# Kernel optimization log

Measured on AMD Instinct MI355X. Metric: run time of the kernel, lower is better.

Reference implementation:

```python
import jax, jax.numpy as jnp
import numpy as np

BINS = 10  # constructor default


def setup_inputs() -> dict:
    key = jax.random.key(0)
    k1, k2 = jax.random.split(key)
    bs, cla = 262144, 128
    # probabilities strictly inside (0,1) so log terms are finite
    u = jax.random.uniform(k1, (bs, cla), dtype=jnp.float32)
    inputs = 0.01 + 0.98 * u
    # binary 0/1 targets as floats
    targets = jnp.round(jax.random.uniform(k2, (bs, cla), dtype=jnp.float32))
    return {"inputs": inputs, "targets": targets}


def reference(inputs, targets):
    bins = BINS
    tot = jnp.asarray(inputs.size, jnp.float32)  # bs * cla

    # gradient-norm proxy g = |p.detach() - t|, in [0, 1]
    g = jnp.abs(jax.lax.stop_gradient(inputs) - targets)

    # edges are i/bins with the last edge nudged to 1+1e-6, so
    # floor(g*bins) clipped to bins-1 reproduces the per-bin masks exactly
    idx = jnp.clip(jnp.floor(g * bins).astype(jnp.int32), 0, bins - 1)

    # histogram counts per bin (fused scatter-add instead of the Python loop)
    counts = jnp.zeros((bins,), jnp.float32).at[idx.ravel()].add(1.0)

    n = jnp.sum(counts > 0).astype(jnp.float32)  # number of non-empty bins
    w_per_bin = jnp.where(counts > 0, tot / jnp.maximum(counts, 1.0), 0.0)
    weights = w_per_bin[idx] / jnp.maximum(n, 1.0)
    weights = jax.lax.stop_gradient(weights)  # weights built from detached g

    # elementwise binary cross entropy on probabilities
    bce = -(targets * jnp.log(inputs) + (1.0 - targets) * jnp.log1p(-inputs))
    loss = jnp.sum(weights * bce) / tot
    return loss
```

## Files before the change

### kernel.cpp

```cpp
#include <hip/hip_runtime.h>

#define BINS 10

__device__ __forceinline__ void elem(float p, float t,
                                     float* __restrict__ sb,
                                     unsigned int* __restrict__ cw)
{
    float g  = fabsf(p - t);
    float l2 = __log2f(1.0f - g);
    int   bi = (int)(g * 10.0f);
#pragma unroll
    for (int b = 0; b < BINS; ++b) {
        bool hit = (bi == b);
        unsigned long long m = __ballot(hit);
        sb[b] += hit ? l2 : 0.0f;
        cw[b] += (unsigned int)__popcll(m);
    }
}

__device__ __forceinline__ void proc8(const float4 pa, const float4 pb,
                                      const float4 ta, const float4 tb,
                                      float* __restrict__ sb,
                                      unsigned int* __restrict__ cw)
{
    elem(pa.x, ta.x, sb, cw); elem(pa.y, ta.y, sb, cw);
    elem(pa.z, ta.z, sb, cw); elem(pa.w, ta.w, sb, cw);
    elem(pb.x, tb.x, sb, cw); elem(pb.y, tb.y, sb, cw);
    elem(pb.z, tb.z, sb, cw); elem(pb.w, tb.w, sb, cw);
}

__global__ __launch_bounds__(256, 4) void ghm_partial(
    const float4* __restrict__ p4,
    const float4* __restrict__ t4,
    float* __restrict__ gsum,
    unsigned int* __restrict__ gcnt,
    int n4)
{
    float        sb[BINS];
    unsigned int cw[BINS];
#pragma unroll
    for (int b = 0; b < BINS; ++b) { sb[b] = 0.0f; cw[b] = 0u; }

    const int tid     = threadIdx.x;
    const int start   = blockIdx.x * blockDim.x + tid;
    const int stride  = gridDim.x * blockDim.x;
    const int stride2 = 2 * stride;
    const int nouter  = n4 / stride2;

    if (nouter >= 2) {
        int i = start;
        float4 pa0 = p4[i], pb0 = p4[i + stride];
        float4 ta0 = t4[i], tb0 = t4[i + stride];
        i += stride2;
        float4 pa1 = p4[i], pb1 = p4[i + stride];
        float4 ta1 = t4[i], tb1 = t4[i + stride];
        i += stride2;
        for (int it = 0; it < nouter - 2; ++it, i += stride2) {
            float4 na = p4[i], nb = p4[i + stride];
            float4 ma = t4[i], mb = t4[i + stride];
            proc8(pa0, pb0, ta0, tb0, sb, cw);
            pa0 = pa1; pb0 = pb1; ta0 = ta1; tb0 = tb1;
            pa1 = na;  pb1 = nb;  ta1 = ma;  tb1 = mb;
        }
        proc8(pa0, pb0, ta0, tb0, sb, cw);
        proc8(pa1, pb1, ta1, tb1, sb, cw);
    } else {
        for (int k = 0; k < 2 * nouter; ++k) {
            int i = start + k * stride;
            float4 p = p4[i], t = t4[i];
            elem(p.x, t.x, sb, cw); elem(p.y, t.y, sb, cw);
            elem(p.z, t.z, sb, cw); elem(p.w, t.w, sb, cw);
        }
    }
    for (int j = start + nouter * stride2; j < n4; j += stride) {
        float4 p = p4[j], t = t4[j];
        elem(p.x, t.x, sb, cw); elem(p.y, t.y, sb, cw);
        elem(p.z, t.z, sb, cw); elem(p.w, t.w, sb, cw);
    }

    __shared__ float        redS[BINS];
    __shared__ unsigned int redC[BINS];
    if (tid < BINS) { redS[tid] = 0.0f; redC[tid] = 0u; }
    __syncthreads();

    const int lane = tid & 63;
#pragma unroll
    for (int b = 0; b < BINS; ++b) {
        float s = sb[b];
#pragma unroll
        for (int off = 32; off > 0; off >>= 1) s += __shfl_down(s, off);
        if (lane == 0) {
            atomicAdd(&redS[b], s);
            atomicAdd(&redC[b], cw[b]);
        }
    }
    __syncthreads();
    if (tid < BINS) {
        atomicAdd(&gsum[tid], redS[tid]);
        atomicAdd(&gcnt[tid], redC[tid]);
    }
}

__global__ void ghm_finalize(const float* __restrict__ gsum,
                             const unsigned int* __restrict__ gcnt,
                             float* __restrict__ out)
{
    if (threadIdx.x == 0 && blockIdx.x == 0) {
        int n = 0;
#pragma unroll
        for (int b = 0; b < BINS; ++b) n += (gcnt[b] > 0u) ? 1 : 0;
        float nn = (float)(n > 0 ? n : 1);
        float acc = 0.0f;
#pragma unroll
        for (int b = 0; b < BINS; ++b) {
            if (gcnt[b] > 0u)
                acc += gsum[b] / ((float)gcnt[b] * nn);
        }
        out[0] = -0.6931471805599453f * acc;
    }
}

extern "C" void kernel_launch(void* const* d_in, const int* in_sizes, int n_in,
                              void* d_out, int out_size, void* d_ws, size_t ws_size,
                              hipStream_t stream)
{
    const float* p = (const float*)d_in[0];
    const float* t = (const float*)d_in[1];
    const int n  = in_sizes[0];
    const int n4 = n >> 2;

    float*        gsum = (float*)d_ws;
    unsigned int* gcnt = (unsigned int*)((char*)d_ws + BINS * sizeof(float));

    hipMemsetAsync(d_ws, 0, BINS * (sizeof(float) + sizeof(unsigned int)), stream);

    const int threads = 256;
    const int blocks  = 2048;
    ghm_partial<<<blocks, threads, 0, stream>>>(
        (const float4*)p, (const float4*)t, gsum, gcnt, n4);

    ghm_finalize<<<1, 64, 0, stream>>>(gsum, gcnt, (float*)d_out);
}
```

Baseline: 293.0 us.

## Replace per-bin ballot loop with per-lane privatized LDS histogram atomics

```diff
diff --git a/kernel.cpp b/kernel.cpp
--- a/kernel.cpp
+++ b/kernel.cpp
@@ -1,32 +1,34 @@
 #include <hip/hip_runtime.h>
 
 #define BINS 10
+#define COPIES 64
+#define HSTRIDE 11
 
 __device__ __forceinline__ void elem(float p, float t,
-                                     float* __restrict__ sb,
-                                     unsigned int* __restrict__ cw)
+                                     float* __restrict__ ssum,
+                                     unsigned int* __restrict__ scnt,
+                                     int lane_off)
 {
     float g  = fabsf(p - t);
     float l2 = __log2f(1.0f - g);
     int   bi = (int)(g * 10.0f);
-#pragma unroll
-    for (int b = 0; b < BINS; ++b) {
-        bool hit = (bi == b);
-        unsigned long long m = __ballot(hit);
-        sb[b] += hit ? l2 : 0.0f;
-        cw[b] += (unsigned int)__popcll(m);
-    }
+    int idx = lane_off + bi;
+    __hip_atomic_fetch_add(&ssum[idx], l2, __ATOMIC_RELAXED,
+                           __HIP_MEMORY_SCOPE_WORKGROUP);
+    __hip_atomic_fetch_add(&scnt[idx], 1u, __ATOMIC_RELAXED,
+                           __HIP_MEMORY_SCOPE_WORKGROUP);
 }
 
 __device__ __forceinline__ void proc8(const float4 pa, const float4 pb,
                                       const float4 ta, const float4 tb,
-                                      float* __restrict__ sb,
-                                      unsigned int* __restrict__ cw)
+                                      float* __restrict__ ssum,
+                                      unsigned int* __restrict__ scnt,
+                                      int lane_off)
 {
-    elem(pa.x, ta.x, sb, cw); elem(pa.y, ta.y, sb, cw);
-    elem(pa.z, ta.z, sb, cw); elem(pa.w, ta.w, sb, cw);
-    elem(pb.x, tb.x, sb, cw); elem(pb.y, tb.y, sb, cw);
-    elem(pb.z, tb.z, sb, cw); elem(pb.w, tb.w, sb, cw);
+    elem(pa.x, ta.x, ssum, scnt, lane_off); elem(pa.y, ta.y, ssum, scnt, lane_off);
+    elem(pa.z, ta.z, ssum, scnt, lane_off); elem(pa.w, ta.w, ssum, scnt, lane_off);
+    elem(pb.x, tb.x, ssum, scnt, lane_off); elem(pb.y, tb.y, ssum, scnt, lane_off);
+    elem(pb.z, tb.z, ssum, scnt, lane_off); elem(pb.w, tb.w, ssum, scnt, lane_off);
 }
 
 __global__ __launch_bounds__(256, 4) void ghm_partial(
@@ -36,16 +38,21 @@
     unsigned int* __restrict__ gcnt,
     int n4)
 {
-    float        sb[BINS];
-    unsigned int cw[BINS];
-#pragma unroll
-    for (int b = 0; b < BINS; ++b) { sb[b] = 0.0f; cw[b] = 0u; }
+    __shared__ float        s_sum[COPIES * HSTRIDE];
+    __shared__ unsigned int s_cnt[COPIES * HSTRIDE];
 
-    const int tid     = threadIdx.x;
-    const int start   = blockIdx.x * blockDim.x + tid;
-    const int stride  = gridDim.x * blockDim.x;
-    const int stride2 = 2 * stride;
-    const int nouter  = n4 / stride2;
+    const int tid = threadIdx.x;
+    for (int k = tid; k < COPIES * HSTRIDE; k += 256) {
+        s_sum[k] = 0.0f;
+        s_cnt[k] = 0u;
+    }
+    __syncthreads();
+
+    const int lane_off = (tid & 63) * HSTRIDE;
+    const int start    = blockIdx.x * blockDim.x + tid;
+    const int stride   = gridDim.x * blockDim.x;
+    const int stride2  = 2 * stride;
+    const int nouter   = n4 / stride2;
 
     if (nouter >= 2) {
         int i = start;
@@ -58,46 +65,43 @@
         for (int it = 0; it < nouter - 2; ++it, i += stride2) {
             float4 na = p4[i], nb = p4[i + stride];
             float4 ma = t4[i], mb = t4[i + stride];
-            proc8(pa0, pb0, ta0, tb0, sb, cw);
+            proc8(pa0, pb0, ta0, tb0, s_sum, s_cnt, lane_off);
             pa0 = pa1; pb0 = pb1; ta0 = ta1; tb0 = tb1;
             pa1 = na;  pb1 = nb;  ta1 = ma;  tb1 = mb;
         }
-        proc8(pa0, pb0, ta0, tb0, sb, cw);
-        proc8(pa1, pb1, ta1, tb1, sb, cw);
+        proc8(pa0, pb0, ta0, tb0, s_sum, s_cnt, lane_off);
+        proc8(pa1, pb1, ta1, tb1, s_sum, s_cnt, lane_off);
     } else {
         for (int k = 0; k < 2 * nouter; ++k) {
             int i = start + k * stride;
             float4 p = p4[i], t = t4[i];
-            elem(p.x, t.x, sb, cw); elem(p.y, t.y, sb, cw);
-            elem(p.z, t.z, sb, cw); elem(p.w, t.w, sb, cw);
+            elem(p.x, t.x, s_sum, s_cnt, lane_off);
+            elem(p.y, t.y, s_sum, s_cnt, lane_off);
+            elem(p.z, t.z, s_sum, s_cnt, lane_off);
+            elem(p.w, t.w, s_sum, s_cnt, lane_off);
         }
     }
     for (int j = start + nouter * stride2; j < n4; j += stride) {
         float4 p = p4[j], t = t4[j];
-        elem(p.x, t.x, sb, cw); elem(p.y, t.y, sb, cw);
-        elem(p.z, t.z, sb, cw); elem(p.w, t.w, sb, cw);
+        elem(p.x, t.x, s_sum, s_cnt, lane_off);
+        elem(p.y, t.y, s_sum, s_cnt, lane_off);
+        elem(p.z, t.z, s_sum, s_cnt, lane_off);
+        elem(p.w, t.w, s_sum, s_cnt, lane_off);
     }
 
-    __shared__ float        redS[BINS];
-    __shared__ unsigned int redC[BINS];
-    if (tid < BINS) { redS[tid] = 0.0f; redC[tid] = 0u; }
-    __syncthreads();
-
-    const int lane = tid & 63;
-#pragma unroll
-    for (int b = 0; b < BINS; ++b) {
-        float s = sb[b];
-#pragma unroll
-        for (int off = 32; off > 0; off >>= 1) s += __shfl_down(s, off);
-        if (lane == 0) {
-            atomicAdd(&redS[b], s);
-            atomicAdd(&redC[b], cw[b]);
-        }
-    }
     __syncthreads();
     if (tid < BINS) {
-        atomicAdd(&gsum[tid], redS[tid]);
-        atomicAdd(&gcnt[tid], redC[tid]);
+        float s = 0.0f;
+#pragma unroll
+        for (int l = 0; l < COPIES; ++l) s += s_sum[l * HSTRIDE + tid];
+        atomicAdd(&gsum[tid], s);
+    }
+    if (tid >= 16 && tid < 16 + BINS) {
+        const int b = tid - 16;
+        unsigned int c = 0u;
+#pragma unroll
+        for (int l = 0; l < COPIES; ++l) c += s_cnt[l * HSTRIDE + b];
+        atomicAdd(&gcnt[b], c);
     }
 }
 
```

Result: slower. 364.2 us (+24.3%).
